# Optimization experiments

Measured on AMD Instinct MI355X. Metric: run time of the kernel, lower is better.

## Reference

```python
import jax, jax.numpy as jnp
import numpy as np
import math

B, NH, DIM = 8, 12, 768
NP, NF = 196, 16            # n (patches per frame), num_frames
DH = DIM // NH              # 64
D3 = 3 * DH                 # per-head feature dim after projection (192)
SEQ = NP * NF               # 3136 body tokens (+1 cls)
ROT = DH                    # rotary dim (RotaryEmbedding(dim=64))
SCALE = 1.0 / (math.sqrt(DH) * NH)


def _heads(t):
    b, s, _ = t.shape
    return t.reshape(b, s, NH, D3).transpose(0, 2, 1, 3)  # b h s d


def _rope(x):
    # lucidrains-style interleaved rotary on the first ROT dims of each head
    s = x.shape[2]
    inv_freq = 1.0 / (10000.0 ** (jnp.arange(0, ROT, 2, dtype=jnp.float32) / ROT))
    freqs = jnp.arange(s, dtype=jnp.float32)[:, None] * inv_freq  # [s, ROT/2]
    freqs = jnp.repeat(freqs, 2, axis=-1)                          # [s, ROT]
    cos, sin = jnp.cos(freqs), jnp.sin(freqs)
    xr, xp = x[..., :ROT], x[..., ROT:]
    x1, x2 = xr[..., ::2], xr[..., 1::2]
    half = jnp.stack((-x2, x1), axis=-1).reshape(xr.shape)
    return jnp.concatenate([xr * cos + half * sin, xp], axis=-1)


def _att_sum(q, k, v):
    # softmax(q k^T * SCALE) v, then sum over queries keepdim (dim 2)
    p = jax.nn.softmax(jnp.einsum('bhqd,bhkd->bhqk', q, k) * SCALE, axis=-1)
    return jnp.einsum('bhqk,bhkd->bhqd', p, v).sum(axis=2, keepdims=True)


def setup_inputs():
    key = jax.random.key(0)
    ks = jax.random.split(key, 11)
    p = lambda k, sh: jax.random.normal(k, sh, jnp.float32) * 0.02
    return {
        'x': jax.random.normal(ks[0], (B, SEQ + 1, DIM), jnp.float32),
        'Wq': p(ks[1], (DIM, 3 * DIM)), 'bq': p(ks[2], (3 * DIM,)),
        'Wk': p(ks[3], (DIM, 3 * DIM)), 'bk': p(ks[4], (3 * DIM,)),
        'Wv': p(ks[5], (DIM, 3 * DIM)), 'bv': p(ks[6], (3 * DIM,)),
        'Wt': p(ks[7], (3 * DIM, DIM)), 'bt': p(ks[8], (DIM,)),
        'Wf': p(ks[9], (3 * DIM, DIM)), 'bf': p(ks[10], (DIM,)),
    }


def reference(x, Wq, bq, Wk, bk, Wv, bv, Wt, bt, Wf, bf):
    body = x[:, 1:, :]
    # NOTE: the original swaps k/v projections for body tokens (k_mat uses self.v, v_mat uses self.k)
    q = _rope(_heads(body @ Wq + bq))
    k = _rope(_heads(body @ Wv + bv))
    v = _heads(body @ Wk + bk)

    # cls-token attention over the full sequence (correct k/v mapping here)
    q_cls = _heads(x[:, 0:1, :] @ Wq + bq)          # [b,h,1,d]
    k_cls = _heads(x @ Wk + bk)
    v_cls = _heads(x @ Wv + bv)
    p_cls = jax.nn.softmax(jnp.einsum('bhqd,bhkd->bhqk', q_cls, k_cls) * SCALE, axis=-1)
    cls_out = jnp.einsum('bhqk,bhkd->bhqd', p_cls, v_cls)  # [b,h,1,d]

    # temporal attention per spatial position x = 1..NP-1, vectorized
    # token index t = f*NP + x  ->  reshape [b,h,NF,NP,d], move spatial first
    qg = q.reshape(B, NH, NF, NP, D3).transpose(0, 1, 3, 2, 4)[:, :, 1:]  # [b,h,NP-1,NF,d]
    kg = k.reshape(B, NH, NF, NP, D3).transpose(0, 1, 3, 2, 4)[:, :, 1:]
    vg = v.reshape(B, NH, NF, NP, D3).transpose(0, 1, 3, 2, 4)[:, :, 1:]
    pg = jax.nn.softmax(jnp.einsum('bhxfd,bhxgd->bhxfg', qg, kg) * SCALE, axis=-1)
    tmp = jnp.einsum('bhxfg,bhxgd->bhxfd', pg, vg).sum(axis=3)  # sum over query frames -> [b,h,NP-1,d]

    temporal = jnp.tile(tmp, (1, 1, NF, 1))  # torch .repeat tiles -> [b,h,(NP-1)*NF,d]
    ti = temporal.transpose(0, 2, 1, 3).reshape(B, (NP - 1) * NF, NH * D3) @ Wt + bt

    # second pass (q uses self.q, v uses self.k, k uses self.v per original)
    q2 = _heads(ti @ Wq + bq)
    v2 = _heads(ti @ Wk + bk)
    k2 = _heads(ti @ Wv + bv)
    outs = [_att_sum(q2[:, :, 0:NP], k2[:, :, 0:NP], v2[:, :, 0:NP])]
    for xi in range(1, NF):  # small fixed loop over frames
        outs.append(_att_sum(q2[:, :, xi:xi + NP], k2[:, :, xi::NP], v2[:, :, xi::NP]))
    t2 = jnp.concatenate(outs, axis=2)        # [b,h,NF,d]
    t2 = jnp.tile(t2, (1, 1, NP, 1))          # [b,h,SEQ,d]
    t2 = jnp.concatenate([cls_out, t2], axis=2)  # [b,h,SEQ+1,d]
    return t2.transpose(0, 2, 1, 3).reshape(B, SEQ + 1, NH * D3) @ Wf + bf
```

## Files before the change

### kernel.cpp

```cpp
#include <hip/hip_runtime.h>
#include <cstdint>
#include <cstddef>


typedef unsigned short u16;
typedef __attribute__((ext_vector_type(8))) short short8;
typedef __attribute__((ext_vector_type(4))) float f32x4;

#define DEV static __device__ __forceinline__
#define AS1 __attribute__((address_space(1)))
#define AS3 __attribute__((address_space(3)))

DEV float b2f(u16 u) { union { unsigned int i; float f; } v; v.i = ((unsigned int)u) << 16; return v.f; }
DEV float b2fs(short s) { return b2f((u16)s); }
DEV u16 f2b(float f) {
    union { float f; unsigned int i; } v; v.f = f;
    unsigned int r = v.i + 0x7fffu + ((v.i >> 16) & 1u);
    return (u16)(r >> 16);
}
DEV void gld16(const u16* g, u16* l) {
    __builtin_amdgcn_global_load_lds((AS1 void*)(g), (AS3 void*)(l), 16, 0, 0);
}

DEV int detect_fl(const u16* x) {
    int lane = threadIdx.x & 63;
    const u16* p = x + lane * 8;
    int c = 0;
#pragma unroll
    for (int j = 0; j < 8; j++) c += (((p[j] >> 7) & 0xFFu) >= 134u);
#pragma unroll
    for (int off = 32; off; off >>= 1) c += __shfl_xor(c, off);
    return c > 8;
}

constexpr int   ROWS  = 3137;
constexpr int   NPm1  = 195;
constexpr int   MT    = 8 * NPm1;
constexpr int   N3    = 2304;
constexpr float SCALE = 1.0f / 96.0f;
constexpr size_t P2Z  = (size_t)MT * N3;
constexpr int   CLS_NS = 32;
constexpr int   CLS_RS = 99;
constexpr int   LDK   = 200;

DEV float wave_max(float v) {
#pragma unroll
    for (int off = 32; off; off >>= 1) v = fmaxf(v, __shfl_xor(v, off));
    return v;
}
DEV float wave_sum(float v) {
#pragma unroll
    for (int off = 32; off; off >>= 1) v += __shfl_xor(v, off);
    return v;
}
DEV float block_max256(float v, float* red) {
    v = wave_max(v);
    __syncthreads();
    if ((threadIdx.x & 63) == 0) red[threadIdx.x >> 6] = v;
    __syncthreads();
    return fmaxf(fmaxf(red[0], red[1]), fmaxf(red[2], red[3]));
}
float __device__ __forceinline__ block_sum256(float v, float* red) {
    v = wave_sum(v);
    __syncthreads();
    if ((threadIdx.x & 63) == 0) red[threadIdx.x >> 6] = v;
    __syncthreads();
    return (red[0] + red[1]) + (red[2] + red[3]);
}

DEV void do_transpose(const void* in, u16* out, int R, int C,
                      int bx, int by, int fl, u16 (*tls)[33]) {
    int tx = threadIdx.x & 31, ty = threadIdx.x >> 5;
#pragma unroll
    for (int i = 0; i < 32; i += 8) {
        int r = by + ty + i, c = bx + tx;
        size_t idx = (size_t)r * C + c;
        tls[ty + i][tx] = fl ? f2b(((const float*)in)[idx]) : ((const u16*)in)[idx];
    }
    __syncthreads();
#pragma unroll
    for (int i = 0; i < 32; i += 8) {
        int c = bx + ty + i, r = by + tx;
        out[(size_t)c * R + r] = tls[tx][ty + i];
    }
}

__global__ __launch_bounds__(256) void prep(const u16* __restrict__ x,
                                            const void* __restrict__ Wq,
                                            const void* __restrict__ Wk,
                                            const void* __restrict__ Wv,
                                            const void* __restrict__ Wt,
                                            const void* __restrict__ Wf,
                                            const void* __restrict__ bq,
                                            const void* __restrict__ bk,
                                            const void* __restrict__ bv,
                                            u16* __restrict__ WT,
                                            u16* __restrict__ WtT,
                                            u16* __restrict__ WfT,
                                            u16* __restrict__ xb,
                                            float* __restrict__ wacc,
                                            float* __restrict__ ropeT,
                                            float* __restrict__ biasF,
                                            int usexb) {
    __shared__ u16 tls[32][33];
    int bid = blockIdx.x;
    if (bid < 5184) {
        int fl = detect_fl(x);
        int z = bid / 1728, t = bid % 1728;
        const void* W = (z == 0) ? Wq : (z == 1) ? Wk : Wv;
        do_transpose(W, WT + (size_t)z * N3 * 768, 768, N3,
                     (t % 72) * 32, (t / 72) * 32, fl, tls);
        return;
    }
    bid -= 5184;
    if (bid < 3456) {
        int fl = detect_fl(x);
        int z = bid / 1728, t = bid % 1728;
        do_transpose(z ? Wf : Wt, z ? WfT : WtT, N3, 768,
                     (t % 24) * 32, (t / 24) * 32, fl, tls);
        return;
    }
    bid -= 3456;
    if (bid < 9411) {
        if (!usexb) return;
        int fl = detect_fl(x);
        size_t e0 = ((size_t)bid * 256 + threadIdx.x) * 8;
        if (fl) {
            const float* p = (const float*)x + e0;
            float4 u0 = *(const float4*)p, u1 = *(const float4*)(p + 4);
            short8 r;
            r[0]=(short)f2b(u0.x); r[1]=(short)f2b(u0.y); r[2]=(short)f2b(u0.z); r[3]=(short)f2b(u0.w);
            r[4]=(short)f2b(u1.x); r[5]=(short)f2b(u1.y); r[6]=(short)f2b(u1.z); r[7]=(short)f2b(u1.w);
            *(short8*)(xb + e0) = r;
        } else {
            *(short8*)(xb + e0) = *(const short8*)(x + e0);
        }
        return;
    }
    bid -= 9411;
    if (bid < 1176) {
        wacc[(size_t)bid * 256 + threadIdx.x] = 0.f;
        return;
    }
    bid -= 1176;
    if (bid < 392) {
        int t = bid * 256 + threadIdx.x;
        int s = t >> 5, i = t & 31;
        float inv = powf(10000.0f, -(float)(2 * i) * (1.0f / 64.0f));
        float sn, cs;
        sincosf((float)s * inv, &sn, &cs);
        ropeT[t * 2]     = cs;
        ropeT[t * 2 + 1] = sn;
        return;
    }
    bid -= 392;
    {
        int fl = detect_fl(x);
        int t = bid * 256 + threadIdx.x;
        int z = t / 2304, i = t - z * 2304;
        const void* b = (z == 0) ? bq : (z == 1) ? bk : bv;
        biasF[t] = fl ? ((const float*)b)[i] : b2f(((const u16*)b)[i]);
    }
}

DEV short8 pack_f32x8(const float* p) {
    const float4 u0 = *(const float4*)p;
    const float4 u1 = *(const float4*)(p + 4);
    short8 r;
    r[0]=(short)f2b(u0.x); r[1]=(short)f2b(u0.y); r[2]=(short)f2b(u0.z); r[3]=(short)f2b(u0.w);
    r[4]=(short)f2b(u1.x); r[5]=(short)f2b(u1.y); r[6]=(short)f2b(u1.z); r[7]=(short)f2b(u1.w);
    return r;
}

__global__ __launch_bounds__(256) void gemm_bt(const void* __restrict__ A, size_t aoff,
                                               const u16* __restrict__ BT,
                                               const void* __restrict__ b0p,
                                               const void* __restrict__ b1p,
                                               const void* __restrict__ b2p,
                                               void* __restrict__ C,
                                               int M, int N, int K,
                                               const u16* __restrict__ xdet,
                                               int araw, int cf32) {
    const int fl = detect_fl(xdet);
    const int af32 = araw && fl;
    const int z = blockIdx.z;
    const u16* Bz = BT + (size_t)z * N * K;
    const void* bias = (z == 0) ? b0p : (z == 1) ? b1p : b2p;

    __shared__ u16 As[128 * 32];
    __shared__ u16 Bs[128 * 32];

    const int tid  = threadIdx.x;
    const int lane = tid & 63;
    const int wave = tid >> 6;
    const int wm   = wave & 1;
    const int wn   = wave >> 1;
    const int quad = lane >> 4;
    const int l16  = lane & 15;

    const int m0 = blockIdx.y * 128;
    const int n0 = blockIdx.x * 128;

    f32x4 acc[4][4] = {};

    if (!af32) {
        const u16* Ab = (const u16*)A + aoff;
        int srow = wave * 32 + (lane >> 2);
        int scol = (lane & 3) * 8;
        int ar0 = m0 + srow;      if (ar0 > M - 1) ar0 = M - 1;
        int ar1 = m0 + srow + 16; if (ar1 > M - 1) ar1 = M - 1;
        const u16* gA0 = Ab + (size_t)ar0 * K + scol;
        const u16* gA1 = Ab + (size_t)ar1 * K + scol;
        const u16* gB0 = Bz + (size_t)(n0 + srow) * K + scol;
        const u16* gB1 = Bz + (size_t)(n0 + srow + 16) * K + scol;
        u16* lA0 = As + wave * 1024;
        u16* lA1 = As + wave * 1024 + 512;
        u16* lB0 = Bs + wave * 1024;
        u16* lB1 = Bs + wave * 1024 + 512;

        for (int k0 = 0; k0 < K; k0 += 32) {
            __syncthreads();
            gld16(gA0 + k0, lA0);
            gld16(gA1 + k0, lA1);
            gld16(gB0 + k0, lB0);
            gld16(gB1 + k0, lB1);
            __syncthreads();

            short8 af[4], bfr[4];
#pragma unroll
            for (int i = 0; i < 4; i++)
                af[i] = *(const short8*)(&As[(wm * 64 + i * 16 + l16) * 32 + quad * 8]);
#pragma unroll
            for (int j = 0; j < 4; j++)
                bfr[j] = *(const short8*)(&Bs[(wn * 64 + j * 16 + l16) * 32 + quad * 8]);
#pragma unroll
            for (int i = 0; i < 4; i++)
#pragma unroll
                for (int j = 0; j < 4; j++)
                    acc[i][j] = __builtin_amdgcn_mfma_f32_16x16x32_bf16(af[i], bfr[j], acc[i][j], 0, 0, 0);
        }
    } else {
        const int r0 = tid >> 2;
        const int kp = (tid & 3) << 3;
        int ga0 = m0 + r0;       if (ga0 > M - 1) ga0 = M - 1;
        int ga1 = m0 + r0 + 64;  if (ga1 > M - 1) ga1 = M - 1;
        const size_t arow0 = aoff + (size_t)ga0 * K + kp;
        const size_t arow1 = aoff + (size_t)ga1 * K + kp;
        const u16* Bp0 = Bz + (size_t)(n0 + r0) * K + kp;
        const u16* Bp1 = Bz + (size_t)(n0 + r0 + 64) * K + kp;

        for (int k0 = 0; k0 < K; k0 += 32) {
            short8 a0 = pack_f32x8((const float*)A + arow0 + k0);
            short8 a1 = pack_f32x8((const float*)A + arow1 + k0);
            short8 bv0 = *(const short8*)(Bp0 + k0);
            short8 bv1 = *(const short8*)(Bp1 + k0);
            __syncthreads();
            *(short8*)(&As[r0 * 32 + kp])        = a0;
            *(short8*)(&As[(r0 + 64) * 32 + kp]) = a1;
            *(short8*)(&Bs[r0 * 32 + kp])        = bv0;
            *(short8*)(&Bs[(r0 + 64) * 32 + kp]) = bv1;
            __syncthreads();

            short8 af[4], bfr[4];
#pragma unroll
            for (int i = 0; i < 4; i++)
                af[i] = *(const short8*)(&As[(wm * 64 + i * 16 + l16) * 32 + quad * 8]);
#pragma unroll
            for (int j = 0; j < 4; j++)
                bfr[j] = *(const short8*)(&Bs[(wn * 64 + j * 16 + l16) * 32 + quad * 8]);
#pragma unroll
            for (int i = 0; i < 4; i++)
#pragma unroll
                for (int j = 0; j < 4; j++)
                    acc[i][j] = __builtin_amdgcn_mfma_f32_16x16x32_bf16(af[i], bfr[j], acc[i][j], 0, 0, 0);
        }
    }

#pragma unroll
    for (int j = 0; j < 4; j++) {
        int col = n0 + wn * 64 + j * 16 + l16;
        float bb = fl ? ((const float*)bias)[col] : b2f(((const u16*)bias)[col]);
#pragma unroll
        for (int i = 0; i < 4; i++) {
            int rowb = m0 + wm * 64 + i * 16 + quad * 4;
#pragma unroll
            for (int r = 0; r < 4; r++) {
                int row = rowb + r;
                if (row < M) {
                    size_t idx = (size_t)z * M * N + (size_t)row * N + col;
                    float v = acc[i][j][r] + bb;
                    if (cf32) ((float*)C)[idx] = v;
                    else      ((u16*)C)[idx]  = f2b(v);
                }
            }
        }
    }
}

__global__ __launch_bounds__(512) void gemm256(const u16* __restrict__ A, size_t aoff,
                                               const u16* __restrict__ BT,
                                               const float* __restrict__ biasF,
                                               u16* __restrict__ C,
                                               int M, int N, int K) {
    __shared__ __align__(16) u16 As[2][16384];
    __shared__ __align__(16) u16 Bs[2][16384];

    const int tid  = threadIdx.x;
    const int lane = tid & 63;
    const int wid  = tid >> 6;
    const int wm   = wid >> 2;
    const int wn   = wid & 3;
    const int quad = lane >> 4;
    const int l16  = lane & 15;
    const int z    = blockIdx.z;

    const int NTN  = N >> 8;
    const int nwg  = gridDim.x;
    const int orig = blockIdx.x;
    const int q8 = nwg >> 3, r8 = nwg & 7, xcd = orig & 7;
    const int wg = (xcd < r8 ? xcd * (q8 + 1) : r8 * (q8 + 1) + (xcd - r8) * q8)
                   + (orig >> 3);
    const int n0 = (wg % NTN) * 256;
    const int m0 = (wg / NTN) * 256;

    const u16* Ab = A + aoff;
    const u16* Bz = BT + (size_t)z * N * K;
    const int  Mc = M - 1;

    const int srow = (wid << 3) + (lane >> 3);
    const int cs   = ((lane & 7) ^ (lane >> 3)) << 3;
    const u16* gA[4]; const u16* gB[4];
#pragma unroll
    for (int h = 0; h < 2; h++)
#pragma unroll
        for (int l = 0; l < 2; l++) {
            int rl = h * 128 + l * 64 + srow;
            int gr = m0 + rl; if (gr > Mc) gr = Mc;
            gA[h * 2 + l] = Ab + (size_t)gr * K + cs;
            gB[h * 2 + l] = Bz + (size_t)(n0 + rl) * K + cs;
        }

    f32x4  acc[8][4] = {};
    short8 aF[4][2], bF[2][2];

    const int rsw  = l16 & 7;
    const int c0   = ((quad ^ rsw) << 3);
    const int c1   = (((4 | quad) ^ rsw) << 3);
    const int aRowB = (wm * 128 + l16) * 64;
    const int bRowB = (wn * 64  + l16) * 64;

#define STG_A(b, h, kt) do { _Pragma("unroll")                                 \
    for (int _l = 0; _l < 2; _l++)                                             \
        gld16(gA[(h) * 2 + _l] + ((kt) << 6),                                  \
              &As[b][(((h) * 128 + _l * 64 + (wid << 3)) << 6)]); } while (0)
#define STG_B(b, h, kt) do { _Pragma("unroll")                                 \
    for (int _l = 0; _l < 2; _l++)                                             \
        gld16(gB[(h) * 2 + _l] + ((kt) << 6),                                  \
              &Bs[b][(((h) * 128 + _l * 64 + (wid << 3)) << 6)]); } while (0)
#define RD_A(b, mh) do { _Pragma("unroll")                                     \
    for (int _m = 0; _m < 4; _m++) {                                           \
        aF[_m][0] = *(const short8*)&As[b][aRowB + (mh) * 4096 + _m * 1024 + c0]; \
        aF[_m][1] = *(const short8*)&As[b][aRowB + (mh) * 4096 + _m * 1024 + c1]; } } while (0)
#define RD_B(b, nh) do { _Pragma("unroll")                                     \
    for (int _n = 0; _n < 2; _n++) {                                           \
        bF[_n][0] = *(const short8*)&Bs[b][bRowB + (nh) * 2048 + _n * 1024 + c0]; \
        bF[_n][1] = *(const short8*)&Bs[b][bRowB + (nh) * 2048 + _n * 1024 + c1]; } } while (0)
#define MM(mh, nh) do {                                                        \
    __builtin_amdgcn_s_setprio(1);                                             \
    _Pragma("unroll") for (int _ks = 0; _ks < 2; _ks++)                        \
    _Pragma("unroll") for (int _m = 0; _m < 4; _m++)                           \
    _Pragma("unroll") for (int _n = 0; _n < 2; _n++)                           \
        acc[(mh) * 4 + _m][(nh) * 2 + _n] =                                    \
            __builtin_amdgcn_mfma_f32_16x16x32_bf16(aF[_m][_ks], bF[_n][_ks],  \
                acc[(mh) * 4 + _m][(nh) * 2 + _n], 0, 0, 0);                   \
    __builtin_amdgcn_s_setprio(0); } while (0)
#define BARR  __builtin_amdgcn_s_barrier()
#define LGKM0 asm volatile("s_waitcnt lgkmcnt(0)" ::: "memory")
#define VMC(n) asm volatile("s_waitcnt vmcnt(" #n ")" ::: "memory")

    STG_A(0, 0, 0); STG_A(0, 1, 0); STG_B(0, 0, 0); STG_B(0, 1, 0);
    STG_A(1, 0, 1);
    VMC(2); BARR;

    const int NP2 = K >> 7;
    for (int i = 0; i < NP2 - 1; i++) {
        const int kt1 = 2 * i + 1, kt2 = 2 * i + 2, kt3 = 2 * i + 3;
        RD_A(0, 0); RD_B(0, 0); STG_A(1, 1, kt1); BARR; LGKM0; MM(0, 0);         BARR;
        RD_B(0, 1);             STG_B(1, 0, kt1); BARR; LGKM0; MM(0, 1);         BARR;
        RD_A(0, 1);             STG_B(1, 1, kt1); BARR; LGKM0; MM(1, 1);         BARR;
        RD_B(0, 0);             STG_A(0, 0, kt2); BARR; LGKM0; MM(1, 0); VMC(2); BARR;
        RD_A(1, 0); RD_B(1, 0); STG_A(0, 1, kt2); BARR; LGKM0; MM(0, 0);         BARR;
        RD_B(1, 1);             STG_B(0, 0, kt2); BARR; LGKM0; MM(0, 1);         BARR;
        RD_A(1, 1);             STG_B(0, 1, kt2); BARR; LGKM0; MM(1, 1);         BARR;
        RD_B(1, 0);             STG_A(1, 0, kt3); BARR; LGKM0; MM(1, 0); VMC(2); BARR;
    }
    {
        const int ktb = 2 * NP2 - 1;
        RD_A(0, 0); RD_B(0, 0); STG_A(1, 1, ktb); BARR; LGKM0; MM(0, 0);         BARR;
        RD_B(0, 1);             STG_B(1, 0, ktb); BARR; LGKM0; MM(0, 1);         BARR;
        RD_A(0, 1);             STG_B(1, 1, ktb); BARR; LGKM0; MM(1, 1);         BARR;
        RD_B(0, 0);                               BARR; LGKM0; MM(1, 0); VMC(0); BARR;
        RD_A(1, 0); RD_B(1, 0);                   BARR; LGKM0; MM(0, 0);         BARR;
        RD_B(1, 1);                               BARR; LGKM0; MM(0, 1);         BARR;
        RD_A(1, 1);                               BARR; LGKM0; MM(1, 1);         BARR;
        RD_B(1, 0);                               BARR; LGKM0; MM(1, 0);
    }
#undef STG_A
#undef STG_B
#undef RD_A
#undef RD_B
#undef MM
#undef BARR
#undef LGKM0
#undef VMC

#pragma unroll
    for (int ni = 0; ni < 4; ni++) {
        int gcol = n0 + wn * 64 + ni * 16 + l16;
        float bb = biasF[z * N + gcol];
#pragma unroll
        for (int mi = 0; mi < 8; mi++) {
            int rowb = m0 + wm * 128 + mi * 16 + quad * 4;
#pragma unroll
            for (int r = 0; r < 4; r++) {
                int row = rowb + r;
                if (row < M)
                    C[(size_t)z * M * N + (size_t)row * N + gcol] =
                        f2b(acc[mi][ni][r] + bb);
            }
        }
    }
}

__global__ __launch_bounds__(256) void phaseA_attn(const u16* __restrict__ Pb, size_t PZv,
                                                   const float* __restrict__ tab,
                                                   u16* __restrict__ tmp,
                                                   float* __restrict__ clsP, int b0) {
    __shared__ __align__(16) char smem[40800];
    int xg = blockIdx.x, h = blockIdx.y, bl = blockIdx.z;
    int b = b0 + bl;
    int tid = threadIdx.x;

    if (xg < 195) {
        int p = xg + 1;
        u16* Qs = (u16*)smem;
        u16* Ks = Qs + 16 * LDK;
        u16* Vs = Ks + 16 * LDK;
        float* w = (float*)(smem + 3 * 16 * LDK * 2);
        const u16* Pq = Pb;
        const u16* Pk = Pb + 2 * PZv;
        const u16* Pv = Pb + PZv;
        const size_t rbase = (size_t)bl * ROWS;

        for (int i = tid; i < 384; i += 256) {
            int f = i / 24, c = (i % 24) * 8;
            int s = f * 196 + p;
            size_t gidx = (rbase + 1 + s) * N3 + (size_t)h * 192 + c;
            short8 q8 = *(const short8*)(Pq + gidx);
            short8 k8 = *(const short8*)(Pk + gidx);
            short8 v8 = *(const short8*)(Pv + gidx);
            if (c < 64) {
                const float* tp = tab + ((size_t)s * 32 + (c >> 1)) * 2;
                float4 t0 = *(const float4*)tp;
                float4 t1 = *(const float4*)(tp + 4);
                float cs[4] = {t0.x, t0.z, t1.x, t1.z};
                float sn[4] = {t0.y, t0.w, t1.y, t1.w};
                short8 qo, ko;
#pragma unroll
                for (int j = 0; j < 4; j++) {
                    float q1 = b2fs(q8[2 * j]), q2 = b2fs(q8[2 * j + 1]);
                    float k1 = b2fs(k8[2 * j]), k2 = b2fs(k8[2 * j + 1]);
                    qo[2 * j]     = (short)f2b(q1 * cs[j] - q2 * sn[j]);
                    qo[2 * j + 1] = (short)f2b(q2 * cs[j] + q1 * sn[j]);
                    ko[2 * j]     = (short)f2b(k1 * cs[j] - k2 * sn[j]);
                    ko[2 * j + 1] = (short)f2b(k2 * cs[j] + k1 * sn[j]);
                }
                q8 = qo; k8 = ko;
            }
            *(short8*)&Qs[f * LDK + c] = q8;
            *(short8*)&Ks[f * LDK + c] = k8;
            *(short8*)&Vs[f * LDK + c] = v8;
        }
        __syncthreads();

        if (tid < 64) {
            int quad = tid >> 4, l16 = tid & 15;
            short8 Af[6], Bf[6];
#pragma unroll
            for (int ks = 0; ks < 6; ks++) {
                Af[ks] = *(const short8*)&Qs[l16 * LDK + quad * 8 + ks * 32];
                Bf[ks] = *(const short8*)&Ks[l16 * LDK + quad * 8 + ks * 32];
            }
            f32x4 S = {0.f, 0.f, 0.f, 0.f};
#pragma unroll
            for (int ks = 0; ks < 6; ks++)
                S = __builtin_amdgcn_mfma_f32_16x16x32_bf16(Af[ks], Bf[ks], S, 0, 0, 0);
            float wcol = 0.f;
#pragma unroll
            for (int r = 0; r < 4; r++) {
                float v = S[r] * SCALE;
                float m = v;
#pragma unroll
                for (int k = 1; k < 16; k <<= 1) m = fmaxf(m, __shfl_xor(m, k));
                float e = __expf(v - m);
                float l = e;
#pragma unroll
                for (int k = 1; k < 16; k <<= 1) l += __shfl_xor(l, k);
                wcol += e / l;
            }
            wcol += __shfl_xor(wcol, 16);
            wcol += __shfl_xor(wcol, 32);
            if (quad == 0) w[l16] = wcol;
        }
        __syncthreads();

        if (tid < 192) {
            float acc = 0.f;
#pragma unroll
            for (int g = 0; g < 16; g++) acc += w[g] * b2f(Vs[g * LDK + tid]);
            tmp[(size_t)(b * NPm1 + p - 1) * N3 + (size_t)h * 192 + tid] = f2b(acc);
        }
    } else {
        int sp = xg - 195;
        int base = sp * CLS_RS;
        int cnt = ROWS - base; if (cnt > CLS_RS) cnt = CLS_RS;
        u16* Ksh  = (u16*)smem;
        float* qs  = (float*)(smem + CLS_RS * LDK * 2);
        float* sc  = qs + 192;
        float* red = sc + 100;
        const size_t hbase = (size_t)bl * ROWS * N3 + (size_t)h * 192;
        const u16* Pq  = Pb;
        const u16* Pkc = Pb + PZv;
        const u16* Pvc = Pb + 2 * PZv;

        if (tid < 192) qs[tid] = b2f(Pq[hbase + tid]);
        for (int i = tid; i < cnt * 24; i += 256) {
            int r = i / 24, c = (i % 24) * 8;
            *(short8*)&Ksh[r * LDK + c] =
                *(const short8*)(Pkc + hbase + (size_t)(base + r) * N3 + c);
        }
        __syncthreads();

        float sval = -1e30f;
        if (tid < cnt) {
            float s = 0.f;
#pragma unroll
            for (int c = 0; c < 24; c++) {
                short8 v8 = *(const short8*)&Ksh[tid * LDK + c * 8];
#pragma unroll
                for (int j = 0; j < 8; j++) s += qs[c * 8 + j] * b2fs(v8[j]);
            }
            sval = s * SCALE;
        }
        float m = block_max256(sval, red);
        float e = (tid < cnt) ? __expf(sval - m) : 0.f;
        float l = block_sum256(e, red);
        if (tid < cnt) sc[tid] = e;
        __syncthreads();

        float* pp = clsP + ((size_t)(b * 12 + h) * CLS_NS + sp) * 194;
        if (tid == 0) { pp[0] = m; pp[1] = l; }
        if (tid < 192) {
            float acc = 0.f;
            const u16* vb = Pvc + hbase + tid;
            for (int r = 0; r < cnt; r++) acc += sc[r] * b2f(vb[(size_t)(base + r) * N3]);
            pp[2 + tid] = acc;
        }
    }
}

__global__ __launch_bounds__(256) void attn2_sc(const u16* __restrict__ P2,
                                                float* __restrict__ wacc) {
    int t = blockIdx.x, h = blockIdx.y, b = blockIdx.z;
    __shared__ u16 Ks[195 * LDK];
    __shared__ u16 Qs[31 * LDK];
    __shared__ float pm[4][16], ps[4][16];
    int tid = threadIdx.x;
    const size_t hb = (size_t)b * NPm1 * N3 + (size_t)h * 192;
    const u16* Q  = P2;
    const u16* Kc = P2 + 2 * P2Z;

    for (int i = tid; i < 195 * 24; i += 256) {
        int r = i / 24, c = (i % 24) * 8;
        *(short8*)&Ks[r * LDK + c] = *(const short8*)(Kc + hb + (size_t)r * N3 + c);
    }
    for (int i = tid; i < 31 * 24; i += 256) {
        int r = i / 24, c = (i % 24) * 8;
        int qr = (t * 16 + r) % 195;
        *(short8*)&Qs[r * LDK + c] = *(const short8*)(Q + hb + (size_t)qr * N3 + c);
    }
    __syncthreads();

    int wave = tid >> 6, lane = tid & 63, quad = lane >> 4, l16 = lane & 15;
    float* wb = wacc + (size_t)((b * 12 + h) * 16) * 196;

    for (int xi = 1 + wave; xi <= 15; xi += 4) {
        short8 Af[6], Bf[6];
#pragma unroll
        for (int ks = 0; ks < 6; ks++) {
            Af[ks] = *(const short8*)&Qs[(xi + l16) * LDK + quad * 8 + ks * 32];
            Bf[ks] = *(const short8*)&Ks[(xi + l16) * LDK + quad * 8 + ks * 32];
        }
        f32x4 S = {0.f, 0.f, 0.f, 0.f};
#pragma unroll
        for (int ks = 0; ks < 6; ks++)
            S = __builtin_amdgcn_mfma_f32_16x16x32_bf16(Af[ks], Bf[ks], S, 0, 0, 0);
        float wcol = 0.f;
#pragma unroll
        for (int r = 0; r < 4; r++) {
            float v = S[r] * SCALE;
            float m = v;
#pragma unroll
            for (int k = 1; k < 16; k <<= 1) m = fmaxf(m, __shfl_xor(m, k));
            float e = __expf(v - m);
            float l = e;
#pragma unroll
            for (int k = 1; k < 16; k <<= 1) l += __shfl_xor(l, k);
            bool qok = (t * 16 + quad * 4 + r) <= 195;
            wcol += qok ? e / l : 0.f;
        }
        wcol += __shfl_xor(wcol, 16);
        wcol += __shfl_xor(wcol, 32);
        if (quad == 0) atomicAdd(&wb[xi * 196 + l16], wcol);
    }

    short8 Af0[6];
#pragma unroll
    for (int ks = 0; ks < 6; ks++)
        Af0[ks] = *(const short8*)&Qs[l16 * LDK + quad * 8 + ks * 32];

    f32x4 Sc[4];
    int   cl[4];
    int   cn = 0;
    for (int c = wave; c < 13; c += 4) {
        int g = c * 16 + l16;
        int krow = g % 195;
        short8 Bf[6];
#pragma unroll
        for (int ks = 0; ks < 6; ks++)
            Bf[ks] = *(const short8*)&Ks[krow * LDK + quad * 8 + ks * 32];
        f32x4 S = {0.f, 0.f, 0.f, 0.f};
#pragma unroll
        for (int ks = 0; ks < 6; ks++)
            S = __builtin_amdgcn_mfma_f32_16x16x32_bf16(Af0[ks], Bf[ks], S, 0, 0, 0);
        bool kbad = g > 195;
#pragma unroll
        for (int r = 0; r < 4; r++) S[r] = kbad ? -1e30f : S[r] * SCALE;
        Sc[cn] = S; cl[cn] = c; cn++;
    }
#pragma unroll
    for (int r = 0; r < 4; r++) {
        float v = -1e30f;
        for (int n = 0; n < cn; n++) v = fmaxf(v, Sc[n][r]);
#pragma unroll
        for (int k = 1; k < 16; k <<= 1) v = fmaxf(v, __shfl_xor(v, k));
        if (l16 == 0) pm[wave][quad * 4 + r] = v;
    }
    __syncthreads();
    float gmx[4], tot[4];
#pragma unroll
    for (int r = 0; r < 4; r++) {
        int qr = quad * 4 + r;
        gmx[r] = fmaxf(fmaxf(pm[0][qr], pm[1][qr]), fmaxf(pm[2][qr], pm[3][qr]));
    }
#pragma unroll
    for (int r = 0; r < 4; r++) {
        float s = 0.f;
        for (int n = 0; n < cn; n++) {
            float e = __expf(Sc[n][r] - gmx[r]);
            Sc[n][r] = e;
            s += e;
        }
#pragma unroll
        for (int k = 1; k < 16; k <<= 1) s += __shfl_xor(s, k);
        if (l16 == 0) ps[wave][quad * 4 + r] = s;
    }
    __syncthreads();
#pragma unroll
    for (int r = 0; r < 4; r++) {
        int qr = quad * 4 + r;
        tot[r] = (ps[0][qr] + ps[1][qr]) + (ps[2][qr] + ps[3][qr]);
    }
    for (int n = 0; n < cn; n++) {
        float wv = 0.f;
#pragma unroll
        for (int r = 0; r < 4; r++) {
            bool qok = (t * 16 + quad * 4 + r) <= 195;
            wv += qok ? Sc[n][r] / tot[r] : 0.f;
        }
        wv += __shfl_xor(wv, 16);
        wv += __shfl_xor(wv, 32);
        int g = cl[n] * 16 + l16;
        if (quad == 0 && g <= 195) atomicAdd(&wb[g], wv);
    }
}

__global__ __launch_bounds__(192) void fin(const u16* __restrict__ P2,
                                           const float* __restrict__ wacc,
                                           const float* __restrict__ clsP,
                                           u16* __restrict__ Fmat) {
    int xg = blockIdx.x, h = blockIdx.y, b = blockIdx.z;
    int tid = threadIdx.x;
    if (xg == 0) {
        const float* p0 = clsP + (size_t)(b * 12 + h) * CLS_NS * 194;
        float M = -1e30f;
#pragma unroll
        for (int s = 0; s < CLS_NS; s++) M = fmaxf(M, p0[s * 194]);
        float L = 0.f, acc = 0.f;
#pragma unroll
        for (int s = 0; s < CLS_NS; s++) {
            float w = __expf(p0[s * 194] - M);
            L += w * p0[s * 194 + 1];
            acc += w * p0[s * 194 + 2 + tid];
        }
        Fmat[(size_t)(b * 17) * N3 + (size_t)h * 192 + tid] = f2b(acc / L);
    } else {
        int xi = xg - 1;
        int Nk = (xi == 0) ? 196 : 16;
        const u16* V = P2 + P2Z;
        const size_t hb = (size_t)b * NPm1 * N3 + (size_t)h * 192;
        const float* wb = wacc + (size_t)((b * 12 + h) * 16 + xi) * 196;
        float acc = 0.f;
        for (int g = 0; g < Nk; g++) {
            int kr = (xi == 0) ? (g % 195) : (xi + g);
            acc += wb[g] * b2f(V[hb + (size_t)kr * N3 + tid]);
        }
        Fmat[(size_t)(b * 17 + 1 + xi) * N3 + (size_t)h * 192 + tid] = f2b(acc);
    }
}

__global__ __launch_bounds__(256) void scatter_out(const float* __restrict__ F17,
                                                   void* __restrict__ out,
                                                   const u16* __restrict__ xdet) {
    const int fl = detect_fl(xdet);
    int t = blockIdx.x * 256 + threadIdx.x;
    int c = t % 96;
    int rem = t / 96;
    int s = rem % ROWS;
    int b = rem / ROWS;
    int src = b * 17 + (s == 0 ? 0 : 1 + ((s - 1) & 15));
    const float* sp = F17 + ((size_t)src * 96 + c) * 8;
    if (fl) {
        float* o = (float*)out + (size_t)t * 8;
        *(float4*)o       = *(const float4*)sp;
        *(float4*)(o + 4) = *(const float4*)(sp + 4);
    } else {
        u16* o = (u16*)out + (size_t)t * 8;
        short8 v;
#pragma unroll
        for (int j = 0; j < 8; j++) v[j] = (short)f2b(sp[j]);
        *(short8*)o = v;
    }
}

extern "C" void kernel_launch(void* const* d_in, const int* in_sizes, int n_in,
                              void* d_out, int out_size, void* d_ws, size_t ws_size,
                              hipStream_t stream) {
    const void* x   = d_in[0];
    const void* Wq  = d_in[1];
    const void* bq  = d_in[2];
    const void* Wk  = d_in[3];
    const void* bk  = d_in[4];
    const void* Wv  = d_in[5];
    const void* bv  = d_in[6];
    const void* Wt  = d_in[7];
    const void* bt  = d_in[8];
    const void* Wf  = d_in[9];
    const void* bfb = d_in[10];
    const u16* xdet = (const u16*)x;
    (void)in_sizes; (void)n_in; (void)out_size;

    auto al = [](size_t b) { return (b + 255) & ~(size_t)255; };
    const size_t szWT   = al((size_t)3 * N3 * 768 * 2);
    const size_t szWtT  = al((size_t)768 * N3 * 2);
    const size_t szTmp  = al((size_t)MT * N3 * 2);
    const size_t szFmat = al((size_t)136 * N3 * 2);
    const size_t szRope = al((size_t)3136 * 32 * 2 * 4);
    const size_t szClsP = al((size_t)8 * 12 * CLS_NS * 194 * 4);
    const size_t szWacc = al((size_t)96 * 16 * 196 * 4);
    const size_t szBias = al((size_t)3 * N3 * 4);
    const size_t szXb   = al((size_t)8 * ROWS * 768 * 2);
    const size_t szB    = al(3 * P2Z * 2) + al((size_t)MT * 768 * 2) +
                          al((size_t)136 * 768 * 4);
    const size_t basePerst = szWT + 2 * szWtT + szTmp + szFmat + szRope +
                             szClsP + szWacc + szBias;

    int bs = 1; int usexb = 0;
    {
        const int cand[4] = {8, 4, 2, 1};
        for (int i = 0; i < 4; i++) {
            size_t szP = al((size_t)3 * cand[i] * ROWS * N3 * 2);
            size_t need = basePerst + szXb + (szP > szB ? szP : szB);
            if (ws_size >= need) { bs = cand[i]; usexb = 1; break; }
        }
        if (!usexb) {
            size_t szP = al((size_t)3 * ROWS * N3 * 2);
            size_t need = basePerst + (szP > szB ? szP : szB);
            if (ws_size < need) return;
        }
    }

    char* ws = (char*)d_ws;
    size_t off = 0;
    auto allocB = [&](size_t bytes) { char* p = ws + off; off += al(bytes); return p; };
    u16*   WT    = (u16*)allocB((size_t)3 * N3 * 768 * 2);
    u16*   WtT   = (u16*)allocB((size_t)768 * N3 * 2);
    u16*   WfT   = (u16*)allocB((size_t)768 * N3 * 2);
    u16*   tmp   = (u16*)allocB((size_t)MT * N3 * 2);
    u16*   Fmat  = (u16*)allocB((size_t)136 * N3 * 2);
    float* ropeT = (float*)allocB((size_t)3136 * 32 * 2 * 4);
    float* clsP  = (float*)allocB((size_t)8 * 12 * CLS_NS * 194 * 4);
    float* wacc  = (float*)allocB((size_t)96 * 16 * 196 * 4);
    float* biasF = (float*)allocB((size_t)3 * N3 * 4);
    u16*   xb    = usexb ? (u16*)allocB((size_t)8 * ROWS * 768 * 2) : nullptr;
    size_t aliasOff = off;
    u16* Pb = (u16*)allocB((size_t)3 * bs * ROWS * N3 * 2);
    off = aliasOff;
    u16*   P2  = (u16*)allocB(3 * P2Z * 2);
    u16*   tiu = (u16*)allocB((size_t)MT * 768 * 2);
    float* F17 = (float*)allocB((size_t)136 * 768 * 4);

    const size_t PZv = (size_t)bs * ROWS * N3;

    prep<<<dim3(19646), 256, 0, stream>>>(xdet, Wq, Wk, Wv, Wt, Wf, bq, bk, bv,
                                          WT, WtT, WfT, xb, wacc, ropeT, biasF,
                                          usexb);

    for (int b0 = 0; b0 < 8; b0 += bs) {
        int Mv = bs * ROWS;
        size_t aoff = (size_t)b0 * ROWS * 768;
        if (usexb) {
            int mtiles = (Mv + 255) >> 8;
            gemm256<<<dim3(9 * mtiles, 1, 3), 512, 0, stream>>>(
                xb, aoff, WT, biasF, Pb, Mv, N3, 768);
        } else {
            gemm_bt<<<dim3(18, (Mv + 127) / 128, 3), 256, 0, stream>>>(
                x, aoff, WT, bq, bk, bv, Pb, Mv, N3, 768, xdet, 1, 0);
        }
        phaseA_attn<<<dim3(227, 12, bs), 256, 0, stream>>>(Pb, PZv, ropeT, tmp, clsP, b0);
    }

    gemm_bt<<<dim3(6, 13, 1), 256, 0, stream>>>(tmp, 0, WtT, bt, bt, bt, tiu,
                                                MT, 768, N3, xdet, 0, 0);
    gemm_bt<<<dim3(18, 13, 3), 256, 0, stream>>>(tiu, 0, WT, bq, bk, bv, P2,
                                                 MT, N3, 768, xdet, 0, 0);
    attn2_sc<<<dim3(13, 12, 8), 256, 0, stream>>>(P2, wacc);
    fin<<<dim3(17, 12, 8), 192, 0, stream>>>(P2, wacc, clsP, Fmat);
    gemm_bt<<<dim3(6, 2, 1), 256, 0, stream>>>(Fmat, 0, WfT, bfb, bfb, bfb, F17,
                                               136, 768, N3, xdet, 0, 1);
    scatter_out<<<dim3(9411), 256, 0, stream>>>(F17, d_out, xdet);
}
```

Measured before the change: 1.145 ms.

## Software-pipeline gemm256 with register double-buffered fragments and fixed K

Rewrites the gemm256 main loop so LDS fragment reads for the next sub-tile are issued before the current MFMA block, using separate fragment register sets (aF0/aF1, bF0a/bF0b/bF1) instead of reading then waiting. K is hardcoded to 768 with 32-bit byte offsets for global-to-LDS loads, the loop is fully specialized to 12 k-tiles, and launch bounds now request 2 blocks per CU. The intent is to overlap LDS reads and global loads with matrix math and cut barrier stalls. The cost is higher register pressure and a kernel that silently breaks for any K other than 768.

```diff
diff --git a/kernel.cpp b/kernel.cpp
--- a/kernel.cpp
+++ b/kernel.cpp
@@ -20,6 +20,9 @@
 }
 DEV void gld16(const u16* g, u16* l) {
     __builtin_amdgcn_global_load_lds((AS1 void*)(g), (AS3 void*)(l), 16, 0, 0);
+}
+DEV void gld16o(const char* gbase, unsigned voff, u16* l) {
+    __builtin_amdgcn_global_load_lds((AS1 void*)(gbase + voff), (AS3 void*)(l), 16, 0, 0);
 }
 
 DEV int detect_fl(const u16* x) {
@@ -297,11 +300,12 @@
     }
 }
 
-__global__ __launch_bounds__(512) void gemm256(const u16* __restrict__ A, size_t aoff,
-                                               const u16* __restrict__ BT,
-                                               const float* __restrict__ biasF,
-                                               u16* __restrict__ C,
-                                               int M, int N, int K) {
+__global__ __launch_bounds__(512, 2) void gemm256(const u16* __restrict__ A, size_t aoff,
+                                                  const u16* __restrict__ BT,
+                                                  const float* __restrict__ biasF,
+                                                  u16* __restrict__ C,
+                                                  int M, int N, int K) {
+    constexpr int KC = 768;
     __shared__ __align__(16) u16 As[2][16384];
     __shared__ __align__(16) u16 Bs[2][16384];
 
@@ -323,92 +327,104 @@
     const int n0 = (wg % NTN) * 256;
     const int m0 = (wg / NTN) * 256;
 
-    const u16* Ab = A + aoff;
-    const u16* Bz = BT + (size_t)z * N * K;
-    const int  Mc = M - 1;
-
-    const int srow = (wid << 3) + (lane >> 3);
-    const int cs   = ((lane & 7) ^ (lane >> 3)) << 3;
-    const u16* gA[4]; const u16* gB[4];
-#pragma unroll
-    for (int h = 0; h < 2; h++)
-#pragma unroll
-        for (int l = 0; l < 2; l++) {
-            int rl = h * 128 + l * 64 + srow;
-            int gr = m0 + rl; if (gr > Mc) gr = Mc;
-            gA[h * 2 + l] = Ab + (size_t)gr * K + cs;
-            gB[h * 2 + l] = Bz + (size_t)(n0 + rl) * K + cs;
-        }
-
-    f32x4  acc[8][4] = {};
-    short8 aF[4][2], bF[2][2];
-
-    const int rsw  = l16 & 7;
-    const int c0   = ((quad ^ rsw) << 3);
-    const int c1   = (((4 | quad) ^ rsw) << 3);
+    const char* Abc = (const char*)(A + aoff);
+    const char* Bbc = (const char*)(BT + (size_t)z * N * KC);
+    const int   Mc  = M - 1;
+
+    const int srow   = (wid << 3) + (lane >> 3);
+    const int cs     = ((lane & 7) ^ (lane >> 3)) << 3;
+    const int wid512 = wid << 9;
+
+    unsigned offA[4];
+#pragma unroll
+    for (int blk = 0; blk < 4; blk++) {
+        int gr = m0 + blk * 64 + srow; if (gr > Mc) gr = Mc;
+        offA[blk] = ((unsigned)gr * KC + (unsigned)cs) * 2u;
+    }
+    const unsigned offB0 = ((unsigned)(n0 + srow) * KC + (unsigned)cs) * 2u;
+    constexpr unsigned BBLK = 64u * KC * 2u;
+
+    f32x4  acc[8][2 * 2] = {};
+    short8 aF0[4][2], aF1[4][2], bF1[2][2], bF0a[2][2], bF0b[2][2];
+
+    const int rsw   = l16 & 7;
+    const int c0    = (quad ^ rsw) << 3;
     const int aRowB = (wm * 128 + l16) * 64;
     const int bRowB = (wn * 64  + l16) * 64;
 
-#define STG_A(b, h, kt) do { _Pragma("unroll")                                 \
-    for (int _l = 0; _l < 2; _l++)                                             \
-        gld16(gA[(h) * 2 + _l] + ((kt) << 6),                                  \
-              &As[b][(((h) * 128 + _l * 64 + (wid << 3)) << 6)]); } while (0)
-#define STG_B(b, h, kt) do { _Pragma("unroll")                                 \
-    for (int _l = 0; _l < 2; _l++)                                             \
-        gld16(gB[(h) * 2 + _l] + ((kt) << 6),                                  \
-              &Bs[b][(((h) * 128 + _l * 64 + (wid << 3)) << 6)]); } while (0)
-#define RD_A(b, mh) do { _Pragma("unroll")                                     \
+#define STG_A02(bi, tt) do {                                                   \
+    gld16o(Abc + (tt) * 128, offA[0], &As[bi][0 * 4096 + wid512]);             \
+    gld16o(Abc + (tt) * 128, offA[2], &As[bi][2 * 4096 + wid512]); } while (0)
+#define STG_A13(bi, tt) do {                                                   \
+    gld16o(Abc + (tt) * 128, offA[1], &As[bi][1 * 4096 + wid512]);             \
+    gld16o(Abc + (tt) * 128, offA[3], &As[bi][3 * 4096 + wid512]); } while (0)
+#define STG_B01(bi, tt) do {                                                   \
+    gld16o(Bbc + (tt) * 128,            offB0, &Bs[bi][0 * 4096 + wid512]);    \
+    gld16o(Bbc + (tt) * 128 + BBLK,     offB0, &Bs[bi][1 * 4096 + wid512]); } while (0)
+#define STG_B23(bi, tt) do {                                                   \
+    gld16o(Bbc + (tt) * 128 + 2 * BBLK, offB0, &Bs[bi][2 * 4096 + wid512]);    \
+    gld16o(Bbc + (tt) * 128 + 3 * BBLK, offB0, &Bs[bi][3 * 4096 + wid512]); } while (0)
+#define RD_A0(bi) do { _Pragma("unroll")                                       \
     for (int _m = 0; _m < 4; _m++) {                                           \
-        aF[_m][0] = *(const short8*)&As[b][aRowB + (mh) * 4096 + _m * 1024 + c0]; \
-        aF[_m][1] = *(const short8*)&As[b][aRowB + (mh) * 4096 + _m * 1024 + c1]; } } while (0)
-#define RD_B(b, nh) do { _Pragma("unroll")                                     \
+        aF0[_m][0] = *(const short8*)&As[bi][aRowB + _m * 1024 + c0];          \
+        aF0[_m][1] = *(const short8*)&As[bi][aRowB + _m * 1024 + (c0 ^ 32)]; } } while (0)
+#define RD_A1(bi) do { _Pragma("unroll")                                       \
+    for (int _m = 0; _m < 4; _m++) {                                           \
+        aF1[_m][0] = *(const short8*)&As[bi][aRowB + 4096 + _m * 1024 + c0];   \
+        aF1[_m][1] = *(const short8*)&As[bi][aRowB + 4096 + _m * 1024 + (c0 ^ 32)]; } } while (0)
+#define RD_B1(bi) do { _Pragma("unroll")                                       \
     for (int _n = 0; _n < 2; _n++) {                                           \
-        bF[_n][0] = *(const short8*)&Bs[b][bRowB + (nh) * 2048 + _n * 1024 + c0]; \
-        bF[_n][1] = *(const short8*)&Bs[b][bRowB + (nh) * 2048 + _n * 1024 + c1]; } } while (0)
-#define MM(mh, nh) do {                                                        \
+        bF1[_n][0] = *(const short8*)&Bs[bi][bRowB + 2048 + _n * 1024 + c0];   \
+        bF1[_n][1] = *(const short8*)&Bs[bi][bRowB + 2048 + _n * 1024 + (c0 ^ 32)]; } } while (0)
+#define RD_B0(bi, SET) do { _Pragma("unroll")                                  \
+    for (int _n = 0; _n < 2; _n++) {                                           \
+        SET[_n][0] = *(const short8*)&Bs[bi][bRowB + _n * 1024 + c0];          \
+        SET[_n][1] = *(const short8*)&Bs[bi][bRowB + _n * 1024 + (c0 ^ 32)]; } } while (0)
+#define MM(AF, BF, mh, nh) do {                                                \
     __builtin_amdgcn_s_setprio(1);                                             \
     _Pragma("unroll") for (int _ks = 0; _ks < 2; _ks++)                        \
     _Pragma("unroll") for (int _m = 0; _m < 4; _m++)                           \
     _Pragma("unroll") for (int _n = 0; _n < 2; _n++)                           \
         acc[(mh) * 4 + _m][(nh) * 2 + _n] =                                    \
-            __builtin_amdgcn_mfma_f32_16x16x32_bf16(aF[_m][_ks], bF[_n][_ks],  \
+            __builtin_amdgcn_mfma_f32_16x16x32_bf16(AF[_m][_ks], BF[_n][_ks],  \
                 acc[(mh) * 4 + _m][(nh) * 2 + _n], 0, 0, 0);                   \
     __builtin_amdgcn_s_setprio(0); } while (0)
 #define BARR  __builtin_amdgcn_s_barrier()
 #define LGKM0 asm volatile("s_waitcnt lgkmcnt(0)" ::: "memory")
 #define VMC(n) asm volatile("s_waitcnt vmcnt(" #n ")" ::: "memory")
 
-    STG_A(0, 0, 0); STG_A(0, 1, 0); STG_B(0, 0, 0); STG_B(0, 1, 0);
-    STG_A(1, 0, 1);
-    VMC(2); BARR;
-
-    const int NP2 = K >> 7;
-    for (int i = 0; i < NP2 - 1; i++) {
-        const int kt1 = 2 * i + 1, kt2 = 2 * i + 2, kt3 = 2 * i + 3;
-        RD_A(0, 0); RD_B(0, 0); STG_A(1, 1, kt1); BARR; LGKM0; MM(0, 0);         BARR;
-        RD_B(0, 1);             STG_B(1, 0, kt1); BARR; LGKM0; MM(0, 1);         BARR;
-        RD_A(0, 1);             STG_B(1, 1, kt1); BARR; LGKM0; MM(1, 1);         BARR;
-        RD_B(0, 0);             STG_A(0, 0, kt2); BARR; LGKM0; MM(1, 0); VMC(2); BARR;
-        RD_A(1, 0); RD_B(1, 0); STG_A(0, 1, kt2); BARR; LGKM0; MM(0, 0);         BARR;
-        RD_B(1, 1);             STG_B(0, 0, kt2); BARR; LGKM0; MM(0, 1);         BARR;
-        RD_A(1, 1);             STG_B(0, 1, kt2); BARR; LGKM0; MM(1, 1);         BARR;
-        RD_B(1, 0);             STG_A(1, 0, kt3); BARR; LGKM0; MM(1, 0); VMC(2); BARR;
-    }
-    {
-        const int ktb = 2 * NP2 - 1;
-        RD_A(0, 0); RD_B(0, 0); STG_A(1, 1, ktb); BARR; LGKM0; MM(0, 0);         BARR;
-        RD_B(0, 1);             STG_B(1, 0, ktb); BARR; LGKM0; MM(0, 1);         BARR;
-        RD_A(0, 1);             STG_B(1, 1, ktb); BARR; LGKM0; MM(1, 1);         BARR;
-        RD_B(0, 0);                               BARR; LGKM0; MM(1, 0); VMC(0); BARR;
-        RD_A(1, 0); RD_B(1, 0);                   BARR; LGKM0; MM(0, 0);         BARR;
-        RD_B(1, 1);                               BARR; LGKM0; MM(0, 1);         BARR;
-        RD_A(1, 1);                               BARR; LGKM0; MM(1, 1);         BARR;
-        RD_B(1, 0);                               BARR; LGKM0; MM(1, 0);
-    }
-#undef STG_A
-#undef STG_B
-#undef RD_A
-#undef RD_B
+    STG_B01(0, 0); STG_B23(0, 0); STG_A02(0, 0); STG_A13(0, 0);
+    STG_B01(1, 1); STG_B23(1, 1); STG_A02(1, 1);
+    VMC(6); BARR;
+    RD_B0(0, bF0a); RD_A0(0);
+
+    for (int i = 0; i < 5; i++) {
+        const int t = 2 * i;
+        RD_B1(0);       STG_A13(1, t + 1); MM(aF0, bF0a, 0, 0); LGKM0;         BARR;
+        RD_A1(0);       STG_B01(0, t + 2); MM(aF0, bF1,  0, 1); LGKM0; VMC(6); BARR;
+        RD_B0(1, bF0b); STG_B23(0, t + 2); MM(aF1, bF1,  1, 1);        VMC(6); BARR;
+        RD_A0(1);       STG_A02(0, t + 2); MM(aF1, bF0a, 1, 0);        VMC(6); BARR;
+        RD_B1(1);       STG_A13(0, t + 2); MM(aF0, bF0b, 0, 0); LGKM0;         BARR;
+        RD_A1(1);       STG_B01(1, t + 3); MM(aF0, bF1,  0, 1); LGKM0; VMC(6); BARR;
+        RD_B0(0, bF0a); STG_B23(1, t + 3); MM(aF1, bF1,  1, 1);        VMC(6); BARR;
+        RD_A0(0);       STG_A02(1, t + 3); MM(aF1, bF0b, 1, 0);        VMC(6); BARR;
+    }
+    RD_B1(0);       STG_A13(1, 11);    MM(aF0, bF0a, 0, 0); LGKM0;         BARR;
+    RD_A1(0);                          MM(aF0, bF1,  0, 1); LGKM0; VMC(4); BARR;
+    RD_B0(1, bF0b);                    MM(aF1, bF1,  1, 1);        VMC(2); BARR;
+    RD_A0(1);                          MM(aF1, bF0a, 1, 0);        VMC(0); BARR;
+    RD_B1(1);                          MM(aF0, bF0b, 0, 0);
+    RD_A1(1);                          MM(aF0, bF1,  0, 1);
+                                       MM(aF1, bF1,  1, 1);
+                                       MM(aF1, bF0b, 1, 0);
+#undef STG_A02
+#undef STG_A13
+#undef STG_B01
+#undef STG_B23
+#undef RD_A0
+#undef RD_A1
+#undef RD_B1
+#undef RD_B0
 #undef MM
 #undef BARR
 #undef LGKM0
```

Result: slower. 1.175 ms (+2.6%).

## Process four patches per block with one wave each, loading Q/K into registers

Applied to the files above, without the earlier changes.

The temporal attention branch of phaseA_attn now assigns one 64-lane wavefront per patch, so a 256-thread block handles four patches instead of one. Q and K fragments are loaded straight from global memory into MFMA registers, and rotary is applied there. Only V is staged in LDS, and the softmax weights are broadcast by shuffle, which removes the block-wide syncthreads and the idle threads. The grid shrinks from 227 to 81 blocks in x, and the CLS-branch index offset is adjusted to match. The cost is global loads that are less coalesced for the MFMA fragments.

```diff
diff --git a/kernel.cpp b/kernel.cpp
--- a/kernel.cpp
+++ b/kernel.cpp
@@ -441,31 +441,45 @@
     int b = b0 + bl;
     int tid = threadIdx.x;
 
-    if (xg < 195) {
-        int p = xg + 1;
-        u16* Qs = (u16*)smem;
-        u16* Ks = Qs + 16 * LDK;
-        u16* Vs = Ks + 16 * LDK;
-        float* w = (float*)(smem + 3 * 16 * LDK * 2);
-        const u16* Pq = Pb;
-        const u16* Pk = Pb + 2 * PZv;
-        const u16* Pv = Pb + PZv;
-        const size_t rbase = (size_t)bl * ROWS;
-
-        for (int i = tid; i < 384; i += 256) {
-            int f = i / 24, c = (i % 24) * 8;
-            int s = f * 196 + p;
-            size_t gidx = (rbase + 1 + s) * N3 + (size_t)h * 192 + c;
-            short8 q8 = *(const short8*)(Pq + gidx);
-            short8 k8 = *(const short8*)(Pk + gidx);
-            short8 v8 = *(const short8*)(Pv + gidx);
-            if (c < 64) {
-                const float* tp = tab + ((size_t)s * 32 + (c >> 1)) * 2;
+    if (xg < 49) {
+        const int wv   = tid >> 6;
+        const int lane = tid & 63;
+        const int p    = xg * 4 + wv + 1;
+        if (p <= 195) {
+            u16* Vw = (u16*)smem + wv * 16 * LDK;
+            const u16* Pq = Pb;
+            const u16* Pk = Pb + 2 * PZv;
+            const u16* Pv = Pb + PZv;
+            const size_t rbase = (size_t)bl * ROWS;
+            const size_t hoff  = (size_t)h * 192;
+
+#pragma unroll
+            for (int rr = 0; rr < 6; rr++) {
+                int idx = rr * 64 + lane;
+                int f = idx / 24, c = (idx % 24) * 8;
+                int s = f * 196 + p;
+                *(short8*)&Vw[f * LDK + c] =
+                    *(const short8*)(Pv + (rbase + 1 + s) * N3 + hoff + c);
+            }
+
+            const int quad = lane >> 4, l16 = lane & 15;
+            const int sQ = l16 * 196 + p;
+            const size_t rowb = (rbase + 1 + sQ) * N3 + hoff;
+            short8 Af[6], Bf[6];
+#pragma unroll
+            for (int ks = 0; ks < 6; ks++) {
+                Af[ks] = *(const short8*)(Pq + rowb + quad * 8 + ks * 32);
+                Bf[ks] = *(const short8*)(Pk + rowb + quad * 8 + ks * 32);
+            }
+#pragma unroll
+            for (int ks = 0; ks < 2; ks++) {
+                int c = quad * 8 + ks * 32;
+                const float* tp = tab + ((size_t)sQ * 32 + (c >> 1)) * 2;
                 float4 t0 = *(const float4*)tp;
                 float4 t1 = *(const float4*)(tp + 4);
                 float cs[4] = {t0.x, t0.z, t1.x, t1.z};
                 float sn[4] = {t0.y, t0.w, t1.y, t1.w};
-                short8 qo, ko;
+                short8 q8 = Af[ks], k8 = Bf[ks], qo, ko;
 #pragma unroll
                 for (int j = 0; j < 4; j++) {
                     float q1 = b2fs(q8[2 * j]), q2 = b2fs(q8[2 * j + 1]);
@@ -475,26 +489,14 @@
                     ko[2 * j]     = (short)f2b(k1 * cs[j] - k2 * sn[j]);
                     ko[2 * j + 1] = (short)f2b(k2 * cs[j] + k1 * sn[j]);
                 }
-                q8 = qo; k8 = ko;
+                Af[ks] = qo; Bf[ks] = ko;
             }
-            *(short8*)&Qs[f * LDK + c] = q8;
-            *(short8*)&Ks[f * LDK + c] = k8;
-            *(short8*)&Vs[f * LDK + c] = v8;
-        }
-        __syncthreads();
-
-        if (tid < 64) {
-            int quad = tid >> 4, l16 = tid & 15;
-            short8 Af[6], Bf[6];
-#pragma unroll
-            for (int ks = 0; ks < 6; ks++) {
-                Af[ks] = *(const short8*)&Qs[l16 * LDK + quad * 8 + ks * 32];
-                Bf[ks] = *(const short8*)&Ks[l16 * LDK + quad * 8 + ks * 32];
-            }
+
             f32x4 S = {0.f, 0.f, 0.f, 0.f};
 #pragma unroll
             for (int ks = 0; ks < 6; ks++)
                 S = __builtin_amdgcn_mfma_f32_16x16x32_bf16(Af[ks], Bf[ks], S, 0, 0, 0);
+
             float wcol = 0.f;
 #pragma unroll
             for (int r = 0; r < 4; r++) {
@@ -510,18 +512,23 @@
             }
             wcol += __shfl_xor(wcol, 16);
             wcol += __shfl_xor(wcol, 32);
-            if (quad == 0) w[l16] = wcol;
-        }
-        __syncthreads();
-
-        if (tid < 192) {
-            float acc = 0.f;
-#pragma unroll
-            for (int g = 0; g < 16; g++) acc += w[g] * b2f(Vs[g * LDK + tid]);
-            tmp[(size_t)(b * NPm1 + p - 1) * N3 + (size_t)h * 192 + tid] = f2b(acc);
+
+            asm volatile("s_waitcnt lgkmcnt(0)" ::: "memory");
+            float a0 = 0.f, a1 = 0.f, a2 = 0.f;
+#pragma unroll
+            for (int g = 0; g < 16; g++) {
+                float wg = __shfl(wcol, g);
+                a0 += wg * b2f(Vw[g * LDK + lane]);
+                a1 += wg * b2f(Vw[g * LDK + lane + 64]);
+                a2 += wg * b2f(Vw[g * LDK + lane + 128]);
+            }
+            u16* op = tmp + (size_t)(b * NPm1 + p - 1) * N3 + hoff;
+            op[lane]       = f2b(a0);
+            op[lane + 64]  = f2b(a1);
+            op[lane + 128] = f2b(a2);
         }
     } else {
-        int sp = xg - 195;
+        int sp = xg - 49;
         int base = sp * CLS_RS;
         int cnt = ROWS - base; if (cnt > CLS_RS) cnt = CLS_RS;
         u16* Ksh  = (u16*)smem;
@@ -837,7 +844,7 @@
             gemm_bt<<<dim3(18, (Mv + 127) / 128, 3), 256, 0, stream>>>(
                 x, aoff, WT, bq, bk, bv, Pb, Mv, N3, 768, xdet, 1, 0);
         }
-        phaseA_attn<<<dim3(227, 12, bs), 256, 0, stream>>>(Pb, PZv, ropeT, tmp, clsP, b0);
+        phaseA_attn<<<dim3(81, 12, bs), 256, 0, stream>>>(Pb, PZv, ropeT, tmp, clsP, b0);
     }
 
     gemm_bt<<<dim3(6, 13, 1), 256, 0, stream>>>(tmp, 0, WtT, bt, bt, bt, tiu,
```

Result: no change. 1.126 ms (-1.6%).
